# Optimization experiments

Hardware: AMD Instinct MI355X
Metric: run time of the kernel (lower is better)

## Reference

```python
import jax, jax.numpy as jnp
import numpy as np

K = 2            # kernel_size
NQ = K * K       # 4 qubits
DEPTH = 1


def _apply1(state, U, q):
    # state: (N,2,2,2,2) complex; apply 2x2 gate U on qubit q
    s = jnp.moveaxis(state, 1 + q, -1)
    s = s @ U.T
    return jnp.moveaxis(s, -1, 1 + q)


def _cnot(state, c, t):
    s = jnp.moveaxis(state, (1 + c, 1 + t), (-2, -1))  # (...,2c,2t)
    s = jnp.stack([s[..., 0, :], s[..., 1, ::-1]], axis=-2)
    return jnp.moveaxis(s, (-2, -1), (1 + c, 1 + t))


def _rx(w):
    c, s = jnp.cos(w / 2), jnp.sin(w / 2)
    return jnp.array([[1, 0], [0, 1]], jnp.complex64) * c + jnp.array([[0, -1j], [-1j, 0]], jnp.complex64) * s


def _ry(w):
    c, s = jnp.cos(w / 2), jnp.sin(w / 2)
    return jnp.array([[1, 0], [0, 1]], jnp.complex64) * c + jnp.array([[0, -1], [1, 0]], jnp.complex64) * s


def setup_inputs() -> dict:
    key = jax.random.key(0)
    k1, k2, k3 = jax.random.split(key, 3)
    B, C, H = 1024, 1, 28
    F = H - K + 1
    n_feat = NQ * C * F * F  # 2916
    x = jax.random.uniform(k1, (B, C, H, H), dtype=jnp.float32)
    W = jax.random.normal(k2, (10, n_feat), dtype=jnp.float32)
    b = jax.random.normal(k3, (10,), dtype=jnp.float32)
    weights = jnp.zeros((DEPTH, NQ), dtype=jnp.float32)  # forward() uses zeros, not the Parameter
    return {"x": x, "W": W, "b": b, "weights": weights}


def reference(x, W, b, weights):
    B, C, H, _ = x.shape
    F = H - K + 1
    # extract all KxK patches, row-major within the patch (matches img[c,i:i+k,j:j+k].reshape(-1))
    p = jnp.stack([x[:, :, i:i + F, j:j + F] for i in range(K) for j in range(K)], axis=-1)  # (B,C,F,F,4)
    ang = p.reshape(-1, NQ) * jnp.pi  # AngleEmbedding angles, (N,4)
    # product state from per-qubit RY(theta)|0> = [cos(t/2), sin(t/2)]
    a = jnp.stack([jnp.cos(ang / 2), jnp.sin(ang / 2)], axis=-1).astype(jnp.complex64)  # (N,4,2)
    state = jnp.einsum('na,nb,nc,nd->nabcd', a[:, 0], a[:, 1], a[:, 2], a[:, 3])
    for l in range(DEPTH):
        w = weights[l]
        state = _apply1(state, _rx(w[0]), 0)
        state = _apply1(state, _rx(w[1]), 1)
        state = _cnot(state, 2, 3)
        state = _cnot(state, 0, 2)
        state = _cnot(state, 0, 3)
        state = _apply1(state, _ry(w[2]), 0)
        state = _apply1(state, _ry(w[3]), 3)
    probs = state.real ** 2 + state.imag ** 2  # (N,2,2,2,2)
    z = jnp.array([1.0, -1.0], dtype=x.dtype)
    evs = []
    for q in range(NQ):
        axes = tuple(ax for ax in range(1, 5) if ax != 1 + q)
        evs.append(probs.sum(axes) @ z)  # <Z_q>, (N,)
    evs = jnp.stack(evs, axis=-1)  # (N, 4)
    # per-image reorder: (C*F*F, 4) -> transpose -> (4*C, F, F)
    q = evs.reshape(B, C, F, F, NQ)
    q = jnp.transpose(q, (0, 4, 1, 2, 3)).reshape(B, NQ * C * F * F)
    return q @ W.T + b
```

## Files before the change

### kernel.cpp

```cpp
#include <hip/hip_runtime.h>


#define HD 28
#define FD 27
#define NPATCH 729
#define NF 2916
#define NG (NF / 4)
#define NOUT 10
#define PSTR 257

__global__ __launch_bounds__(256)
void hqnn_fused(const float* __restrict__ x,
                const float* __restrict__ W,
                const float* __restrict__ bias,
                const float* __restrict__ wts,
                float* __restrict__ out)
{
    __shared__ float sc[HD * HD];
    __shared__ float ss[HD * HD];
    __shared__ __align__(16) float evl[NF];
    __shared__ float part[NOUT * PSTR];

    const int b   = blockIdx.x;
    const int tid = threadIdx.x;

    const float w0 = wts[0], w1 = wts[1], w2 = wts[2], w3 = wts[3];
    const float cw0 = cosf(w0);
    const float cw1 = cosf(w1);
    const float cw2 = cosf(w2), sw2 = sinf(w2);
    const float cw3 = cosf(w3), sw3 = sinf(w3);

    const float4* xb4 = (const float4*)(x + b * (HD * HD));
    if (tid < 196) {
        const float4 v = xb4[tid];
        float s0, c0, s1, c1, s2, c2, s3, c3;
        sincospif(v.x, &s0, &c0);
        sincospif(v.y, &s1, &c1);
        sincospif(v.z, &s2, &c2);
        sincospif(v.w, &s3, &c3);
        const int p4 = tid * 4;
        sc[p4] = c0; sc[p4 + 1] = c1; sc[p4 + 2] = c2; sc[p4 + 3] = c3;
        ss[p4] = s0; ss[p4 + 1] = s1; ss[p4 + 2] = s2; ss[p4 + 3] = s3;
    }
    __syncthreads();

    for (int pp = tid; pp < NPATCH; pp += 256) {
        const int fi = pp / FD;
        const int fj = pp - fi * FD;
        const int p  = fi * HD + fj;

        const float c00 = sc[p];
        const float c01 = sc[p + 1];
        const float c10 = sc[p + HD];
        const float c11 = sc[p + HD + 1];
        const float s00 = ss[p];
        const float s10 = ss[p + HD];
        const float s11 = ss[p + HD + 1];

        const float ev2 = cw0 * c00 * c10;
        evl[pp]               = cw2 * cw0 * c00 - sw2 * s00 * s10;
        evl[NPATCH + pp]      = cw1 * c01;
        evl[2 * NPATCH + pp]  = ev2;
        evl[3 * NPATCH + pp]  = cw3 * ev2 * c11 - sw3 * s11;
    }
    __syncthreads();

    float acc[NOUT];
#pragma unroll
    for (int o = 0; o < NOUT; ++o) acc[o] = 0.f;

    const float4* W4  = (const float4*)W;
    const float4* ev4 = (const float4*)evl;
    for (int g = tid; g < NG; g += 256) {
        const float4 e = ev4[g];
#pragma unroll
        for (int o = 0; o < NOUT; ++o) {
            const float4 w = W4[o * NG + g];
            acc[o] += e.x * w.x + e.y * w.y + e.z * w.z + e.w * w.w;
        }
    }

#pragma unroll
    for (int o = 0; o < NOUT; ++o) part[o * PSTR + tid] = acc[o];
    __syncthreads();

    if (tid < NOUT * 16) {
        const int o = tid >> 4;
        const int j = tid & 15;
        float s = 0.f;
#pragma unroll
        for (int k = 0; k < 256; k += 16) s += part[o * PSTR + j + k];
        s += __shfl_down(s, 8, 16);
        s += __shfl_down(s, 4, 16);
        s += __shfl_down(s, 2, 16);
        s += __shfl_down(s, 1, 16);
        if (j == 0) out[b * NOUT + o] = s + bias[o];
    }
}

extern "C" void kernel_launch(void* const* d_in, const int* in_sizes, int n_in,
                              void* d_out, int out_size, void* d_ws, size_t ws_size,
                              hipStream_t stream) {
    const float* x    = (const float*)d_in[0];
    const float* W    = (const float*)d_in[1];
    const float* bias = (const float*)d_in[2];
    const float* wts  = (const float*)d_in[3];
    float* out = (float*)d_out;

    const int B = in_sizes[0] / (HD * HD);
    hqnn_fused<<<B, 256, 0, stream>>>(x, W, bias, wts, out);
}
```

Baseline: 66.75 us.

## Process two images per block to reuse W loads across images

Each block now handles two images instead of one, so every float4 of W read from global memory feeds two dot products. Shared-memory buffers for the sin/cos tables and the reduction partials share space through a union to keep LDS usage in check. The grid halves to 512 blocks, which cuts W traffic per image but leaves fewer blocks to spread across CUs and doubles register accumulators. B is assumed to be even.

```diff
diff --git a/kernel.cpp b/kernel.cpp
--- a/kernel.cpp
+++ b/kernel.cpp
@@ -2,12 +2,14 @@
 
 
 #define HD 28
+#define NPIX 784
 #define FD 27
 #define NPATCH 729
 #define NF 2916
-#define NG (NF / 4)
+#define NG 729
 #define NOUT 10
 #define PSTR 257
+#define IM 2
 
 __global__ __launch_bounds__(256)
 void hqnn_fused(const float* __restrict__ x,
@@ -16,12 +18,12 @@
                 const float* __restrict__ wts,
                 float* __restrict__ out)
 {
-    __shared__ float sc[HD * HD];
-    __shared__ float ss[HD * HD];
-    __shared__ __align__(16) float evl[NF];
-    __shared__ float part[NOUT * PSTR];
+    __shared__ __align__(16) float evl[IM][NF];
+    __shared__ union U {
+        struct { float sc[IM][NPIX]; float ss[IM][NPIX]; } tr;
+        float part[IM * NOUT][PSTR];
+    } u;
 
-    const int b   = blockIdx.x;
     const int tid = threadIdx.x;
 
     const float w0 = wts[0], w1 = wts[1], w2 = wts[2], w3 = wts[3];
@@ -30,71 +32,87 @@
     const float cw2 = cosf(w2), sw2 = sinf(w2);
     const float cw3 = cosf(w3), sw3 = sinf(w3);
 
-    const float4* xb4 = (const float4*)(x + b * (HD * HD));
-    if (tid < 196) {
-        const float4 v = xb4[tid];
+    const float4* xb4 = (const float4*)(x + blockIdx.x * (IM * NPIX));
+    for (int t = tid; t < IM * NPIX / 4; t += 256) {
+        const float4 v = xb4[t];
+        const int p4  = t * 4;
+        const int img = (p4 >= NPIX) ? 1 : 0;
+        const int off = p4 - img * NPIX;
         float s0, c0, s1, c1, s2, c2, s3, c3;
         sincospif(v.x, &s0, &c0);
         sincospif(v.y, &s1, &c1);
         sincospif(v.z, &s2, &c2);
         sincospif(v.w, &s3, &c3);
-        const int p4 = tid * 4;
-        sc[p4] = c0; sc[p4 + 1] = c1; sc[p4 + 2] = c2; sc[p4 + 3] = c3;
-        ss[p4] = s0; ss[p4 + 1] = s1; ss[p4 + 2] = s2; ss[p4 + 3] = s3;
+        u.tr.sc[img][off]     = c0; u.tr.ss[img][off]     = s0;
+        u.tr.sc[img][off + 1] = c1; u.tr.ss[img][off + 1] = s1;
+        u.tr.sc[img][off + 2] = c2; u.tr.ss[img][off + 2] = s2;
+        u.tr.sc[img][off + 3] = c3; u.tr.ss[img][off + 3] = s3;
     }
     __syncthreads();
 
-    for (int pp = tid; pp < NPATCH; pp += 256) {
-        const int fi = pp / FD;
-        const int fj = pp - fi * FD;
-        const int p  = fi * HD + fj;
+    for (int pp = tid; pp < IM * NPATCH; pp += 256) {
+        const int img = pp / NPATCH;
+        const int pa  = pp - img * NPATCH;
+        const int fi  = pa / FD;
+        const int fj  = pa - fi * FD;
+        const int p   = fi * HD + fj;
 
-        const float c00 = sc[p];
-        const float c01 = sc[p + 1];
-        const float c10 = sc[p + HD];
-        const float c11 = sc[p + HD + 1];
-        const float s00 = ss[p];
-        const float s10 = ss[p + HD];
-        const float s11 = ss[p + HD + 1];
+        const float c00 = u.tr.sc[img][p];
+        const float c01 = u.tr.sc[img][p + 1];
+        const float c10 = u.tr.sc[img][p + HD];
+        const float c11 = u.tr.sc[img][p + HD + 1];
+        const float s00 = u.tr.ss[img][p];
+        const float s10 = u.tr.ss[img][p + HD];
+        const float s11 = u.tr.ss[img][p + HD + 1];
 
         const float ev2 = cw0 * c00 * c10;
-        evl[pp]               = cw2 * cw0 * c00 - sw2 * s00 * s10;
-        evl[NPATCH + pp]      = cw1 * c01;
-        evl[2 * NPATCH + pp]  = ev2;
-        evl[3 * NPATCH + pp]  = cw3 * ev2 * c11 - sw3 * s11;
+        evl[img][pa]               = cw2 * cw0 * c00 - sw2 * s00 * s10;
+        evl[img][NPATCH + pa]      = cw1 * c01;
+        evl[img][2 * NPATCH + pa]  = ev2;
+        evl[img][3 * NPATCH + pa]  = cw3 * ev2 * c11 - sw3 * s11;
     }
     __syncthreads();
 
-    float acc[NOUT];
+    float acc[IM][NOUT];
 #pragma unroll
-    for (int o = 0; o < NOUT; ++o) acc[o] = 0.f;
+    for (int m = 0; m < IM; ++m)
+#pragma unroll
+        for (int o = 0; o < NOUT; ++o) acc[m][o] = 0.f;
 
-    const float4* W4  = (const float4*)W;
-    const float4* ev4 = (const float4*)evl;
+    const float4* W4 = (const float4*)W;
+    const float4* e0 = (const float4*)evl[0];
+    const float4* e1 = (const float4*)evl[1];
     for (int g = tid; g < NG; g += 256) {
-        const float4 e = ev4[g];
+        const float4 a = e0[g];
+        const float4 c = e1[g];
 #pragma unroll
         for (int o = 0; o < NOUT; ++o) {
             const float4 w = W4[o * NG + g];
-            acc[o] += e.x * w.x + e.y * w.y + e.z * w.z + e.w * w.w;
+            acc[0][o] += a.x * w.x + a.y * w.y + a.z * w.z + a.w * w.w;
+            acc[1][o] += c.x * w.x + c.y * w.y + c.z * w.z + c.w * w.w;
         }
     }
 
 #pragma unroll
-    for (int o = 0; o < NOUT; ++o) part[o * PSTR + tid] = acc[o];
+    for (int m = 0; m < IM; ++m)
+#pragma unroll
+        for (int o = 0; o < NOUT; ++o) u.part[m * NOUT + o][tid] = acc[m][o];
     __syncthreads();
 
-    if (tid < NOUT * 16) {
-        const int o = tid >> 4;
-        const int j = tid & 15;
+    if (tid < IM * NOUT * 8) {
+        const int row = tid >> 3;
+        const int j   = tid & 7;
         float s = 0.f;
 #pragma unroll
-        for (int k = 0; k < 256; k += 16) s += part[o * PSTR + j + k];
-        s += __shfl_down(s, 8, 16);
-        s += __shfl_down(s, 4, 16);
-        s += __shfl_down(s, 2, 16);
-        s += __shfl_down(s, 1, 16);
-        if (j == 0) out[b * NOUT + o] = s + bias[o];
+        for (int k = 0; k < 256; k += 8) s += u.part[row][j + k];
+        s += __shfl_down(s, 4, 8);
+        s += __shfl_down(s, 2, 8);
+        s += __shfl_down(s, 1, 8);
+        if (j == 0) {
+            const int img = (row >= NOUT) ? 1 : 0;
+            const int o   = row - img * NOUT;
+            out[(blockIdx.x * IM + img) * NOUT + o] = s + bias[o];
+        }
     }
 }
 
@@ -107,6 +125,6 @@
     const float* wts  = (const float*)d_in[3];
     float* out = (float*)d_out;
 
-    const int B = in_sizes[0] / (HD * HD);
-    hqnn_fused<<<B, 256, 0, stream>>>(x, W, bias, wts, out);
+    const int B = in_sizes[0] / NPIX;
+    hqnn_fused<<<B / IM, 256, 0, stream>>>(x, W, bias, wts, out);
 }
```

Result: faster. 65.28 us (median of 2 runs) (-2.2%).
